# Performance work log

Measured on AMD Instinct MI355X. Metric: run time of the kernel, lower is better.

## Reference

```python
import jax, jax.numpy as jnp
import numpy as np

N_NODES = 50000
N_EDGES = 800000
F_NODE = 64
F_EDGE = 32
F_GLOBAL = 32
OUT_DIM = 64
N_GRAPHS = 256


def setup_inputs() -> dict:
    key = jax.random.key(0)
    ks = jax.random.split(key, 8)
    x = jax.random.normal(ks[0], (N_NODES, F_NODE), dtype=jnp.float32)
    edge_index = jax.random.randint(ks[1], (2, N_EDGES), 0, N_NODES, dtype=jnp.int64)
    edge_attr = jax.random.normal(ks[2], (N_EDGES, F_EDGE), dtype=jnp.float32)
    u = jax.random.normal(ks[3], (N_GRAPHS, F_GLOBAL), dtype=jnp.float32)
    batch = jnp.sort(jax.random.randint(ks[4], (N_NODES,), 0, N_GRAPHS, dtype=jnp.int64))
    # params (scaled like default Linear init)
    W1 = jax.random.normal(ks[5], (F_NODE + F_EDGE, OUT_DIM), dtype=jnp.float32) / np.sqrt(F_NODE + F_EDGE)
    b1 = jnp.zeros((OUT_DIM,), dtype=jnp.float32)
    W2 = jax.random.normal(ks[6], (F_NODE + OUT_DIM + F_GLOBAL, OUT_DIM), dtype=jnp.float32) / np.sqrt(F_NODE + OUT_DIM + F_GLOBAL)
    b2 = jnp.zeros((OUT_DIM,), dtype=jnp.float32)
    return {"x": x, "edge_index": edge_index, "edge_attr": edge_attr,
            "u": u, "batch": batch, "W1": W1, "b1": b1, "W2": W2, "b2": b2}


def reference(x, edge_index, edge_attr, u, batch, W1, b1, W2, b2):
    dest, src = edge_index[0], edge_index[1]
    # gather source node features + edge attrs -> [E, F_NODE + F_EDGE]
    edge_info = jnp.concatenate([x[src], edge_attr], axis=1)
    # node_mlp_1: Linear + ReLU
    edge_messages = jax.nn.relu(edge_info @ W1 + b1)  # [E, OUT_DIM]
    # scatter-sum into destination nodes
    aggregated = jax.ops.segment_sum(edge_messages, dest, num_segments=x.shape[0])  # [N, OUT_DIM]
    # concat node, aggregated messages, per-graph global
    node_info = jnp.concatenate([x, aggregated, u[batch]], axis=1)  # [N, F_NODE+OUT_DIM+F_GLOBAL]
    # node_mlp_2: Linear + ReLU
    return jax.nn.relu(node_info @ W2 + b2)  # [N, OUT_DIM]
```

## Files before the change

kernel.cpp:

```cpp
#include <hip/hip_runtime.h>
#include <hip/hip_bf16.h>
#include <hip/hip_fp16.h>

typedef __attribute__((ext_vector_type(8))) short short8;
typedef __attribute__((ext_vector_type(4))) float f32x4;

constexpr int NN = 50000;
constexpr int NE = 800000;
constexpr int FN = 64;
constexpr int FE = 32;
constexpr int FG = 32;
constexpr int OD = 64;
constexpr int NG = 256;

constexpr int SCAN_B = 256;
constexpr int NBLK = (NN + SCAN_B - 1) / SCAN_B;

constexpr int NWIN_E = NE / 16;
constexpr int MS_BLOCKS = 2048;
constexpr int MS_WAVES  = MS_BLOCKS * 4;
constexpr int NWIN_N = NN / 16;
constexpr int NODE_BLOCKS = 782;
constexpr int NODE_WAVES  = NODE_BLOCKS * 4;

static __device__ __forceinline__ unsigned pack_bf16(float a, float b) {
    __hip_bfloat162 h = __float22bfloat162_rn(float2{a, b});
    return *reinterpret_cast<unsigned*>(&h);
}

__global__ __launch_bounds__(256) void k_xcvt(const float* __restrict__ x,
                                              unsigned* __restrict__ xb32) {
    const int i = blockIdx.x * 256 + threadIdx.x;
    if (i >= NN * FN / 8) return;
    const float4* p = (const float4*)(x + (size_t)i * 8);
    float4 f0 = p[0], f1 = p[1];
    uint4 o;
    o.x = pack_bf16(f0.x, f0.y);
    o.y = pack_bf16(f0.z, f0.w);
    o.z = pack_bf16(f1.x, f1.y);
    o.w = pack_bf16(f1.z, f1.w);
    ((uint4*)xb32)[i] = o;
}

__global__ __launch_bounds__(256) void k_uw2(const float* __restrict__ u,
                                             const float* __restrict__ W2,
                                             const float* __restrict__ b2,
                                             float* __restrict__ uW2b) {
    const int lane = threadIdx.x & 63;
    float wcol[FG];
#pragma unroll
    for (int k = 0; k < FG; ++k) wcol[k] = W2[(FN + OD + k) * OD + lane];
    const float bias = b2[lane];

    int g = (blockIdx.x * blockDim.x + threadIdx.x) >> 6;
    g = __builtin_amdgcn_readfirstlane(g);
    if (g >= NG) return;

    const float* __restrict__ urow = u + (size_t)g * FG;
    float acc = bias;
#pragma unroll
    for (int k = 0; k < FG; ++k) acc = fmaf(urow[k], wcol[k], acc);
    uW2b[(size_t)g * OD + lane] = acc;
}

__global__ __launch_bounds__(256) void k_hist(const int* __restrict__ ei,
                                              int* __restrict__ cnt) {
    const int e = blockIdx.x * blockDim.x + threadIdx.x;
    if (e < NE) atomicAdd(&cnt[ei[e]], 1);
}

__global__ __launch_bounds__(SCAN_B) void k_scan1(const int* __restrict__ cnt,
                                                  int* __restrict__ start,
                                                  int* __restrict__ bsum) {
    __shared__ int lds[SCAN_B];
    const int i = blockIdx.x * SCAN_B + threadIdx.x;
    const int v = (i < NN) ? cnt[i] : 0;
    lds[threadIdx.x] = v;
    __syncthreads();
#pragma unroll
    for (int off = 1; off < SCAN_B; off <<= 1) {
        int t = (threadIdx.x >= off) ? lds[threadIdx.x - off] : 0;
        __syncthreads();
        lds[threadIdx.x] += t;
        __syncthreads();
    }
    const int incl = lds[threadIdx.x];
    if (i < NN) start[i] = incl - v;
    if (threadIdx.x == SCAN_B - 1) bsum[blockIdx.x] = incl;
}

__global__ __launch_bounds__(SCAN_B) void k_scan2(const int* __restrict__ bsum,
                                                  int* __restrict__ bscan) {
    __shared__ int lds[SCAN_B];
    const int i = threadIdx.x;
    const int v = (i < NBLK) ? bsum[i] : 0;
    lds[i] = v;
    __syncthreads();
#pragma unroll
    for (int off = 1; off < SCAN_B; off <<= 1) {
        int t = (i >= off) ? lds[i - off] : 0;
        __syncthreads();
        lds[i] += t;
        __syncthreads();
    }
    if (i < NBLK) bscan[i] = lds[i] - v;
}

__global__ __launch_bounds__(SCAN_B) void k_scan3(int* __restrict__ start,
                                                  const int* __restrict__ bscan,
                                                  const int* __restrict__ cnt,
                                                  int* __restrict__ cursor) {
    const int i = blockIdx.x * SCAN_B + threadIdx.x;
    if (i < NN) {
        const int s = start[i] + bscan[blockIdx.x];
        start[i] = s;
        cursor[i] = s;
        if (i == NN - 1) start[NN] = s + cnt[i];
    }
}

__global__ __launch_bounds__(256) void k_msgscat(const int* __restrict__ ei,
                                                 const float* __restrict__ ea,
                                                 const unsigned short* __restrict__ xb,
                                                 const float* __restrict__ W1,
                                                 const float* __restrict__ b1,
                                                 int* __restrict__ cursor,
                                                 unsigned short* __restrict__ mbuf) {
    const int l = threadIdx.x & 63;
    const int g = l >> 4;
    const int c = l & 15;

    short8 wf[3][4];
#pragma unroll
    for (int t = 0; t < 3; ++t)
#pragma unroll
        for (int b = 0; b < 4; ++b)
#pragma unroll
            for (int i = 0; i < 8; i += 2) {
                const int k = 32 * t + 8 * g + i;
                const unsigned p = pack_bf16(W1[k * OD + (c + 16 * b)],
                                             W1[(k + 1) * OD + (c + 16 * b)]);
                ((unsigned*)&wf[t][b])[i / 2] = p;
            }
    float bias[4];
#pragma unroll
    for (int b = 0; b < 4; ++b) bias[b] = b1[c + 16 * b];

    int wv = (blockIdx.x * blockDim.x + threadIdx.x) >> 6;
    wv = __builtin_amdgcn_readfirstlane(wv);

    for (int w = wv; w < NWIN_E; w += MS_WAVES) {
        const int e = w * 16 + c;
        const int dst = ei[e];
        const int src = ei[NE + e];
        int pos = 0;
        if (l < 16) pos = atomicAdd(&cursor[dst], 1);

        short8 a0, a1, a2;
        {
            const uint4* xr = (const uint4*)(xb + (size_t)src * FN);
            uint4 q0 = xr[g];
            uint4 q1 = xr[4 + g];
            a0 = *(short8*)&q0;
            a1 = *(short8*)&q1;
        }
        {
            const float4* er = (const float4*)(ea + (size_t)e * FE);
            float4 e0 = er[2 * g], e1 = er[2 * g + 1];
            uint4 q2;
            q2.x = pack_bf16(e0.x, e0.y);
            q2.y = pack_bf16(e0.z, e0.w);
            q2.z = pack_bf16(e1.x, e1.y);
            q2.w = pack_bf16(e1.z, e1.w);
            a2 = *(short8*)&q2;
        }

        f32x4 accb[4];
#pragma unroll
        for (int b = 0; b < 4; ++b) {
            f32x4 acc = {0.f, 0.f, 0.f, 0.f};
            acc = __builtin_amdgcn_mfma_f32_16x16x32_bf16(a0, wf[0][b], acc, 0, 0, 0);
            acc = __builtin_amdgcn_mfma_f32_16x16x32_bf16(a1, wf[1][b], acc, 0, 0, 0);
            acc = __builtin_amdgcn_mfma_f32_16x16x32_bf16(a2, wf[2][b], acc, 0, 0, 0);
            accb[b] = acc;
        }

#pragma unroll
        for (int q = 0; q < 4; ++q) {
            const int pr = __shfl(pos, 4 * g + q);
            const float v0 = fmaxf(accb[0][q] + bias[0], 0.0f);
            const float v1 = fmaxf(accb[1][q] + bias[1], 0.0f);
            const float v2 = fmaxf(accb[2][q] + bias[2], 0.0f);
            const float v3 = fmaxf(accb[3][q] + bias[3], 0.0f);
            const __half2 h01 = __float22half2_rn(float2{v0, v1});
            const __half2 h23 = __float22half2_rn(float2{v2, v3});
            uint2 out;
            out.x = *reinterpret_cast<const unsigned*>(&h01);
            out.y = *reinterpret_cast<const unsigned*>(&h23);
            *reinterpret_cast<uint2*>(mbuf + (size_t)pr * 64 + c * 4) = out;
        }
    }
}

__global__ __launch_bounds__(256) void k_segred(const unsigned short* __restrict__ mbuf,
                                                const int* __restrict__ start,
                                                unsigned short* __restrict__ aggb) {
    const int l = threadIdx.x & 63;
    int n = (blockIdx.x * blockDim.x + threadIdx.x) >> 6;
    n = __builtin_amdgcn_readfirstlane(n);
    if (n >= NN) return;

    const int r0 = start[n];
    const int r1 = start[n + 1];
    const __half* mh = (const __half*)mbuf;

    float s0 = 0.0f, s1 = 0.0f, s2 = 0.0f, s3 = 0.0f;
    int r = r0;
    for (; r + 3 < r1; r += 4) {
        s0 += __half2float(mh[(size_t)(r + 0) * 64 + l]);
        s1 += __half2float(mh[(size_t)(r + 1) * 64 + l]);
        s2 += __half2float(mh[(size_t)(r + 2) * 64 + l]);
        s3 += __half2float(mh[(size_t)(r + 3) * 64 + l]);
    }
    for (; r < r1; ++r) s0 += __half2float(mh[(size_t)r * 64 + l]);
    const float s = (s0 + s1) + (s2 + s3);

    const int tc = (l >> 2) + 16 * (l & 3);
    __hip_bfloat16 hb = __float2bfloat16(s);
    aggb[(size_t)n * OD + tc] = *reinterpret_cast<unsigned short*>(&hb);
}

__global__ __launch_bounds__(256) void k_nodem(const unsigned short* __restrict__ xb,
                                               const unsigned short* __restrict__ aggb,
                                               const int* __restrict__ bat,
                                               const float* __restrict__ uW2b,
                                               const float* __restrict__ W2,
                                               float* __restrict__ out) {
    const int l = threadIdx.x & 63;
    const int g = l >> 4;
    const int c = l & 15;

    short8 wf[4][4];
#pragma unroll
    for (int t = 0; t < 4; ++t)
#pragma unroll
        for (int b = 0; b < 4; ++b)
#pragma unroll
            for (int i = 0; i < 8; i += 2) {
                const int k = 32 * t + 8 * g + i;
                const unsigned p = pack_bf16(W2[k * OD + (c + 16 * b)],
                                             W2[(k + 1) * OD + (c + 16 * b)]);
                ((unsigned*)&wf[t][b])[i / 2] = p;
            }

    int wv = (blockIdx.x * blockDim.x + threadIdx.x) >> 6;
    wv = __builtin_amdgcn_readfirstlane(wv);

    for (int w = wv; w < NWIN_N; w += NODE_WAVES) {
        const int n0 = w * 16;
        const uint4* xr = (const uint4*)(xb + (size_t)(n0 + c) * FN);
        const uint4* ar = (const uint4*)(aggb + (size_t)(n0 + c) * OD);
        uint4 qx0 = xr[g], qx1 = xr[4 + g];
        uint4 qa0 = ar[g], qa1 = ar[4 + g];
        short8 a0 = *(short8*)&qx0, a1 = *(short8*)&qx1;
        short8 a2 = *(short8*)&qa0, a3 = *(short8*)&qa1;

        int bq[4];
#pragma unroll
        for (int q = 0; q < 4; ++q) bq[q] = bat[n0 + g * 4 + q];

#pragma unroll
        for (int b = 0; b < 4; ++b) {
            f32x4 acc = {0.f, 0.f, 0.f, 0.f};
            acc = __builtin_amdgcn_mfma_f32_16x16x32_bf16(a0, wf[0][b], acc, 0, 0, 0);
            acc = __builtin_amdgcn_mfma_f32_16x16x32_bf16(a1, wf[1][b], acc, 0, 0, 0);
            acc = __builtin_amdgcn_mfma_f32_16x16x32_bf16(a2, wf[2][b], acc, 0, 0, 0);
            acc = __builtin_amdgcn_mfma_f32_16x16x32_bf16(a3, wf[3][b], acc, 0, 0, 0);
#pragma unroll
            for (int q = 0; q < 4; ++q) {
                const int n = n0 + g * 4 + q;
                const float val = acc[q] + uW2b[(size_t)bq[q] * OD + c + 16 * b];
                out[(size_t)n * OD + c + 16 * b] = fmaxf(val, 0.0f);
            }
        }
    }
}

extern "C" void kernel_launch(void* const* d_in, const int* in_sizes, int n_in,
                              void* d_out, int out_size, void* d_ws, size_t ws_size,
                              hipStream_t stream) {
    const float* x    = (const float*)d_in[0];
    const int*   ei   = (const int*)d_in[1];
    const float* ea   = (const float*)d_in[2];
    const float* u    = (const float*)d_in[3];
    const int*   bat  = (const int*)d_in[4];
    const float* W1   = (const float*)d_in[5];
    const float* b1   = (const float*)d_in[6];
    const float* W2   = (const float*)d_in[7];
    const float* b2   = (const float*)d_in[8];
    float* out = (float*)d_out;

    char* ws = (char*)d_ws;
    auto alloc = [&](size_t bytes) {
        char* p = ws;
        ws += (bytes + 255) & ~size_t(255);
        return p;
    };
    unsigned short* xb   = (unsigned short*)alloc((size_t)NN * FN * 2);
    unsigned short* aggb = (unsigned short*)alloc((size_t)NN * OD * 2);
    float* uW2b    = (float*)alloc((size_t)NG * OD * sizeof(float));
    int*   cnt     = (int*)alloc((size_t)NN * sizeof(int));
    int*   start   = (int*)alloc((size_t)(NN + 1) * sizeof(int));
    int*   cursor  = (int*)alloc((size_t)NN * sizeof(int));
    int*   bsum    = (int*)alloc((size_t)NBLK * sizeof(int));
    int*   bscan   = (int*)alloc((size_t)NBLK * sizeof(int));
    unsigned short* mbuf = (unsigned short*)alloc((size_t)NE * OD * 2);

    hipMemsetAsync(cnt, 0, (size_t)NN * sizeof(int), stream);

    k_xcvt<<<dim3((NN * FN / 8 + 255) / 256), dim3(256), 0, stream>>>(x, (unsigned*)xb);
    k_uw2<<<dim3((NG * 64 + 255) / 256), dim3(256), 0, stream>>>(u, W2, b2, uW2b);

    k_hist<<<dim3((NE + 255) / 256), dim3(256), 0, stream>>>(ei, cnt);
    k_scan1<<<dim3(NBLK), dim3(SCAN_B), 0, stream>>>(cnt, start, bsum);
    k_scan2<<<dim3(1), dim3(SCAN_B), 0, stream>>>(bsum, bscan);
    k_scan3<<<dim3(NBLK), dim3(SCAN_B), 0, stream>>>(start, bscan, cnt, cursor);

    k_msgscat<<<dim3(MS_BLOCKS), dim3(256), 0, stream>>>(ei, ea, xb, W1, b1, cursor, mbuf);

    k_segred<<<dim3((NN * 64 + 255) / 256), dim3(256), 0, stream>>>(mbuf, start, aggb);

    k_nodem<<<dim3(NODE_BLOCKS), dim3(256), 0, stream>>>(xb, aggb, bat, uW2b, W2, out);
}
```

Measured before the change: 154.6 us.

## Precompute CSR slots in separate kernel; vectorize segment reduction with half2 loads

Moves the per-edge atomic cursor increment out of the MFMA message kernel into a new dedicated kernel that writes a slot index per edge. The message kernel then reads precomputed slots instead of doing atomics and shuffles. The segment reduction now loads half2 pairs, with two half-waves each taking alternate rows. This leaves the aggregate in a permuted column order, which is compensated by permuting the W2 rows loaded in the node kernel. The cost is an extra kernel launch plus writing and reading a 3.2MB slot array.

```diff
diff --git a/kernel.cpp b/kernel.cpp
--- a/kernel.cpp
+++ b/kernel.cpp
@@ -119,12 +119,22 @@
     }
 }
 
+__global__ __launch_bounds__(256) void k_slot(const int* __restrict__ ei,
+                                              int* __restrict__ cursor,
+                                              int* __restrict__ slotb) {
+    const int e = blockIdx.x * blockDim.x + threadIdx.x;
+    if (e < NE) {
+        const int pos = atomicAdd(&cursor[ei[e]], 1);
+        slotb[e] = pos;
+    }
+}
+
 __global__ __launch_bounds__(256) void k_msgscat(const int* __restrict__ ei,
                                                  const float* __restrict__ ea,
                                                  const unsigned short* __restrict__ xb,
                                                  const float* __restrict__ W1,
                                                  const float* __restrict__ b1,
-                                                 int* __restrict__ cursor,
+                                                 const int* __restrict__ slotb,
                                                  unsigned short* __restrict__ mbuf) {
     const int l = threadIdx.x & 63;
     const int g = l >> 4;
@@ -151,10 +161,11 @@
 
     for (int w = wv; w < NWIN_E; w += MS_WAVES) {
         const int e = w * 16 + c;
-        const int dst = ei[e];
         const int src = ei[NE + e];
-        int pos = 0;
-        if (l < 16) pos = atomicAdd(&cursor[dst], 1);
+
+        int pr[4];
+#pragma unroll
+        for (int q = 0; q < 4; ++q) pr[q] = slotb[w * 16 + 4 * g + q];
 
         short8 a0, a1, a2;
         {
@@ -187,7 +198,6 @@
 
 #pragma unroll
         for (int q = 0; q < 4; ++q) {
-            const int pr = __shfl(pos, 4 * g + q);
             const float v0 = fmaxf(accb[0][q] + bias[0], 0.0f);
             const float v1 = fmaxf(accb[1][q] + bias[1], 0.0f);
             const float v2 = fmaxf(accb[2][q] + bias[2], 0.0f);
@@ -197,37 +207,44 @@
             uint2 out;
             out.x = *reinterpret_cast<const unsigned*>(&h01);
             out.y = *reinterpret_cast<const unsigned*>(&h23);
-            *reinterpret_cast<uint2*>(mbuf + (size_t)pr * 64 + c * 4) = out;
-        }
-    }
-}
-
-__global__ __launch_bounds__(256) void k_segred(const unsigned short* __restrict__ mbuf,
+            *reinterpret_cast<uint2*>(mbuf + (size_t)pr[q] * 64 + c * 4) = out;
+        }
+    }
+}
+
+__global__ __launch_bounds__(256) void k_segred(const unsigned* __restrict__ mb32,
                                                 const int* __restrict__ start,
-                                                unsigned short* __restrict__ aggb) {
+                                                unsigned* __restrict__ aggb32) {
     const int l = threadIdx.x & 63;
+    const int half = l >> 5;
+    const int q = l & 31;
     int n = (blockIdx.x * blockDim.x + threadIdx.x) >> 6;
     n = __builtin_amdgcn_readfirstlane(n);
     if (n >= NN) return;
 
     const int r0 = start[n];
     const int r1 = start[n + 1];
-    const __half* mh = (const __half*)mbuf;
-
-    float s0 = 0.0f, s1 = 0.0f, s2 = 0.0f, s3 = 0.0f;
+
+    float c0 = 0.0f, c1 = 0.0f;
     int r = r0;
-    for (; r + 3 < r1; r += 4) {
-        s0 += __half2float(mh[(size_t)(r + 0) * 64 + l]);
-        s1 += __half2float(mh[(size_t)(r + 1) * 64 + l]);
-        s2 += __half2float(mh[(size_t)(r + 2) * 64 + l]);
-        s3 += __half2float(mh[(size_t)(r + 3) * 64 + l]);
-    }
-    for (; r < r1; ++r) s0 += __half2float(mh[(size_t)r * 64 + l]);
-    const float s = (s0 + s1) + (s2 + s3);
-
-    const int tc = (l >> 2) + 16 * (l & 3);
-    __hip_bfloat16 hb = __float2bfloat16(s);
-    aggb[(size_t)n * OD + tc] = *reinterpret_cast<unsigned short*>(&hb);
+#pragma unroll 4
+    for (; r + 1 < r1; r += 2) {
+        const unsigned uu = mb32[(size_t)(r + half) * 32 + q];
+        const __half2 h = *reinterpret_cast<const __half2*>(&uu);
+        const float2 f = __half22float2(h);
+        c0 += f.x;
+        c1 += f.y;
+    }
+    if (r < r1 && half == 0) {
+        const unsigned uu = mb32[(size_t)r * 32 + q];
+        const __half2 h = *reinterpret_cast<const __half2*>(&uu);
+        const float2 f = __half22float2(h);
+        c0 += f.x;
+        c1 += f.y;
+    }
+    c0 += __shfl_xor(c0, 32);
+    c1 += __shfl_xor(c1, 32);
+    if (half == 0) aggb32[(size_t)n * 32 + q] = pack_bf16(c0, c1);
 }
 
 __global__ __launch_bounds__(256) void k_nodem(const unsigned short* __restrict__ xb,
@@ -247,9 +264,18 @@
         for (int b = 0; b < 4; ++b)
 #pragma unroll
             for (int i = 0; i < 8; i += 2) {
-                const int k = 32 * t + 8 * g + i;
-                const unsigned p = pack_bf16(W2[k * OD + (c + 16 * b)],
-                                             W2[(k + 1) * OD + (c + 16 * b)]);
+                const int col = c + 16 * b;
+                unsigned p;
+                if (t < 2) {
+                    const int k = 32 * t + 8 * g + i;
+                    p = pack_bf16(W2[k * OD + col], W2[(k + 1) * OD + col]);
+                } else {
+                    const int sc0 = 32 * (t - 2) + 8 * g + i;
+                    const int sc1 = sc0 + 1;
+                    const int k0 = FN + ((sc0 >> 2) + 16 * (sc0 & 3));
+                    const int k1 = FN + ((sc1 >> 2) + 16 * (sc1 & 3));
+                    p = pack_bf16(W2[k0 * OD + col], W2[k1 * OD + col]);
+                }
                 ((unsigned*)&wf[t][b])[i / 2] = p;
             }
 
@@ -314,6 +340,7 @@
     int*   cursor  = (int*)alloc((size_t)NN * sizeof(int));
     int*   bsum    = (int*)alloc((size_t)NBLK * sizeof(int));
     int*   bscan   = (int*)alloc((size_t)NBLK * sizeof(int));
+    int*   slotb   = (int*)alloc((size_t)NE * sizeof(int));
     unsigned short* mbuf = (unsigned short*)alloc((size_t)NE * OD * 2);
 
     hipMemsetAsync(cnt, 0, (size_t)NN * sizeof(int), stream);
@@ -325,10 +352,11 @@
     k_scan1<<<dim3(NBLK), dim3(SCAN_B), 0, stream>>>(cnt, start, bsum);
     k_scan2<<<dim3(1), dim3(SCAN_B), 0, stream>>>(bsum, bscan);
     k_scan3<<<dim3(NBLK), dim3(SCAN_B), 0, stream>>>(start, bscan, cnt, cursor);
-
-    k_msgscat<<<dim3(MS_BLOCKS), dim3(256), 0, stream>>>(ei, ea, xb, W1, b1, cursor, mbuf);
-
-    k_segred<<<dim3((NN * 64 + 255) / 256), dim3(256), 0, stream>>>(mbuf, start, aggb);
+    k_slot<<<dim3((NE + 255) / 256), dim3(256), 0, stream>>>(ei, cursor, slotb);
+
+    k_msgscat<<<dim3(MS_BLOCKS), dim3(256), 0, stream>>>(ei, ea, xb, W1, b1, slotb, mbuf);
+
+    k_segred<<<dim3((NN * 64 + 255) / 256), dim3(256), 0, stream>>>((const unsigned*)mbuf, start, (unsigned*)aggb);
 
     k_nodem<<<dim3(NODE_BLOCKS), dim3(256), 0, stream>>>(xb, aggb, bat, uW2b, W2, out);
 }
```

Result: slower. 179.5 us (+16.1%).

## Fuse segment reduction into node MLP and merge small preprocessing kernels

Applied to the files above, without the earlier changes.

Removes the separate segment-reduce kernel. Each node-MLP wave now sums its 16 nodes' fp16 messages directly from the sorted message buffer into bf16 MFMA operands, and the W2 aggregate rows are permuted to match the lane layout. The x conversion, u·W2 precompute and count zeroing are merged into one kernel, and the two scan tail kernels become one that rescans the block sums redundantly in every block. This cuts launches and the aggregate write/read round trip. The cost is load imbalance inside each wave, since every node's loop runs to the maximum degree among its 16 nodes.

```diff
diff --git a/kernel.cpp b/kernel.cpp
--- a/kernel.cpp
+++ b/kernel.cpp
@@ -19,6 +19,10 @@
 constexpr int NWIN_E = NE / 16;
 constexpr int MS_BLOCKS = 2048;
 constexpr int MS_WAVES  = MS_BLOCKS * 4;
+
+constexpr int XCVT_BLOCKS = (NN * FN / 8 + 255) / 256;
+constexpr int PRE_BLOCKS  = XCVT_BLOCKS + (NG * 64) / 256;
+
 constexpr int NWIN_N = NN / 16;
 constexpr int NODE_BLOCKS = 782;
 constexpr int NODE_WAVES  = NODE_BLOCKS * 4;
@@ -28,9 +32,31 @@
     return *reinterpret_cast<unsigned*>(&h);
 }
 
-__global__ __launch_bounds__(256) void k_xcvt(const float* __restrict__ x,
-                                              unsigned* __restrict__ xb32) {
+__global__ __launch_bounds__(256) void k_pre(const float* __restrict__ x,
+                                             unsigned* __restrict__ xb32,
+                                             const float* __restrict__ u,
+                                             const float* __restrict__ W2,
+                                             const float* __restrict__ b2,
+                                             float* __restrict__ uW2b,
+                                             int* __restrict__ cnt) {
+    if (blockIdx.x >= XCVT_BLOCKS) {
+        const int lane = threadIdx.x & 63;
+        float wcol[FG];
+#pragma unroll
+        for (int k = 0; k < FG; ++k) wcol[k] = W2[(FN + OD + k) * OD + lane];
+        const float bias = b2[lane];
+        int g = ((blockIdx.x - XCVT_BLOCKS) * 256 + threadIdx.x) >> 6;
+        g = __builtin_amdgcn_readfirstlane(g);
+        if (g >= NG) return;
+        const float* __restrict__ urow = u + (size_t)g * FG;
+        float acc = bias;
+#pragma unroll
+        for (int k = 0; k < FG; ++k) acc = fmaf(urow[k], wcol[k], acc);
+        uW2b[(size_t)g * OD + lane] = acc;
+        return;
+    }
     const int i = blockIdx.x * 256 + threadIdx.x;
+    if (i < NN) cnt[i] = 0;
     if (i >= NN * FN / 8) return;
     const float4* p = (const float4*)(x + (size_t)i * 8);
     float4 f0 = p[0], f1 = p[1];
@@ -42,27 +68,6 @@
     ((uint4*)xb32)[i] = o;
 }
 
-__global__ __launch_bounds__(256) void k_uw2(const float* __restrict__ u,
-                                             const float* __restrict__ W2,
-                                             const float* __restrict__ b2,
-                                             float* __restrict__ uW2b) {
-    const int lane = threadIdx.x & 63;
-    float wcol[FG];
-#pragma unroll
-    for (int k = 0; k < FG; ++k) wcol[k] = W2[(FN + OD + k) * OD + lane];
-    const float bias = b2[lane];
-
-    int g = (blockIdx.x * blockDim.x + threadIdx.x) >> 6;
-    g = __builtin_amdgcn_readfirstlane(g);
-    if (g >= NG) return;
-
-    const float* __restrict__ urow = u + (size_t)g * FG;
-    float acc = bias;
-#pragma unroll
-    for (int k = 0; k < FG; ++k) acc = fmaf(urow[k], wcol[k], acc);
-    uW2b[(size_t)g * OD + lane] = acc;
-}
-
 __global__ __launch_bounds__(256) void k_hist(const int* __restrict__ ei,
                                               int* __restrict__ cnt) {
     const int e = blockIdx.x * blockDim.x + threadIdx.x;
@@ -89,30 +94,26 @@
     if (threadIdx.x == SCAN_B - 1) bsum[blockIdx.x] = incl;
 }
 
-__global__ __launch_bounds__(SCAN_B) void k_scan2(const int* __restrict__ bsum,
-                                                  int* __restrict__ bscan) {
+__global__ __launch_bounds__(SCAN_B) void k_scan23(int* __restrict__ start,
+                                                   const int* __restrict__ bsum,
+                                                   const int* __restrict__ cnt,
+                                                   int* __restrict__ cursor) {
     __shared__ int lds[SCAN_B];
-    const int i = threadIdx.x;
-    const int v = (i < NBLK) ? bsum[i] : 0;
-    lds[i] = v;
+    const int t = threadIdx.x;
+    lds[t] = (t < NBLK) ? bsum[t] : 0;
     __syncthreads();
 #pragma unroll
     for (int off = 1; off < SCAN_B; off <<= 1) {
-        int t = (i >= off) ? lds[i - off] : 0;
+        int tv = (t >= off) ? lds[t - off] : 0;
         __syncthreads();
-        lds[i] += t;
+        lds[t] += tv;
         __syncthreads();
     }
-    if (i < NBLK) bscan[i] = lds[i] - v;
-}
-
-__global__ __launch_bounds__(SCAN_B) void k_scan3(int* __restrict__ start,
-                                                  const int* __restrict__ bscan,
-                                                  const int* __restrict__ cnt,
-                                                  int* __restrict__ cursor) {
-    const int i = blockIdx.x * SCAN_B + threadIdx.x;
+    const int boff = (blockIdx.x == 0) ? 0 : lds[blockIdx.x - 1];
+
+    const int i = blockIdx.x * SCAN_B + t;
     if (i < NN) {
-        const int s = start[i] + bscan[blockIdx.x];
+        const int s = start[i] + boff;
         start[i] = s;
         cursor[i] = s;
         if (i == NN - 1) start[NN] = s + cnt[i];
@@ -194,48 +195,21 @@
             const float v3 = fmaxf(accb[3][q] + bias[3], 0.0f);
             const __half2 h01 = __float22half2_rn(float2{v0, v1});
             const __half2 h23 = __float22half2_rn(float2{v2, v3});
-            uint2 out;
-            out.x = *reinterpret_cast<const unsigned*>(&h01);
-            out.y = *reinterpret_cast<const unsigned*>(&h23);
-            *reinterpret_cast<uint2*>(mbuf + (size_t)pr * 64 + c * 4) = out;
-        }
-    }
-}
-
-__global__ __launch_bounds__(256) void k_segred(const unsigned short* __restrict__ mbuf,
+            uint2 outv;
+            outv.x = *reinterpret_cast<const unsigned*>(&h01);
+            outv.y = *reinterpret_cast<const unsigned*>(&h23);
+            *reinterpret_cast<uint2*>(mbuf + (size_t)pr * 64 + c * 4) = outv;
+        }
+    }
+}
+
+__global__ __launch_bounds__(256) void k_nodem2(const unsigned short* __restrict__ xb,
+                                                const unsigned short* __restrict__ mbuf,
                                                 const int* __restrict__ start,
-                                                unsigned short* __restrict__ aggb) {
-    const int l = threadIdx.x & 63;
-    int n = (blockIdx.x * blockDim.x + threadIdx.x) >> 6;
-    n = __builtin_amdgcn_readfirstlane(n);
-    if (n >= NN) return;
-
-    const int r0 = start[n];
-    const int r1 = start[n + 1];
-    const __half* mh = (const __half*)mbuf;
-
-    float s0 = 0.0f, s1 = 0.0f, s2 = 0.0f, s3 = 0.0f;
-    int r = r0;
-    for (; r + 3 < r1; r += 4) {
-        s0 += __half2float(mh[(size_t)(r + 0) * 64 + l]);
-        s1 += __half2float(mh[(size_t)(r + 1) * 64 + l]);
-        s2 += __half2float(mh[(size_t)(r + 2) * 64 + l]);
-        s3 += __half2float(mh[(size_t)(r + 3) * 64 + l]);
-    }
-    for (; r < r1; ++r) s0 += __half2float(mh[(size_t)r * 64 + l]);
-    const float s = (s0 + s1) + (s2 + s3);
-
-    const int tc = (l >> 2) + 16 * (l & 3);
-    __hip_bfloat16 hb = __float2bfloat16(s);
-    aggb[(size_t)n * OD + tc] = *reinterpret_cast<unsigned short*>(&hb);
-}
-
-__global__ __launch_bounds__(256) void k_nodem(const unsigned short* __restrict__ xb,
-                                               const unsigned short* __restrict__ aggb,
-                                               const int* __restrict__ bat,
-                                               const float* __restrict__ uW2b,
-                                               const float* __restrict__ W2,
-                                               float* __restrict__ out) {
+                                                const int* __restrict__ bat,
+                                                const float* __restrict__ uW2b,
+                                                const float* __restrict__ W2,
+                                                float* __restrict__ out) {
     const int l = threadIdx.x & 63;
     const int g = l >> 4;
     const int c = l & 15;
@@ -247,9 +221,18 @@
         for (int b = 0; b < 4; ++b)
 #pragma unroll
             for (int i = 0; i < 8; i += 2) {
-                const int k = 32 * t + 8 * g + i;
-                const unsigned p = pack_bf16(W2[k * OD + (c + 16 * b)],
-                                             W2[(k + 1) * OD + (c + 16 * b)]);
+                const int col = c + 16 * b;
+                unsigned p;
+                if (t < 2) {
+                    const int k = 32 * t + 8 * g + i;
+                    p = pack_bf16(W2[k * OD + col], W2[(k + 1) * OD + col]);
+                } else {
+                    const int sc0 = 32 * (t - 2) + 8 * g + i;
+                    const int sc1 = sc0 + 1;
+                    const int k0 = FN + ((sc0 >> 2) + 16 * (sc0 & 3));
+                    const int k1 = FN + ((sc1 >> 2) + 16 * (sc1 & 3));
+                    p = pack_bf16(W2[k0 * OD + col], W2[k1 * OD + col]);
+                }
                 ((unsigned*)&wf[t][b])[i / 2] = p;
             }
 
@@ -258,12 +241,50 @@
 
     for (int w = wv; w < NWIN_N; w += NODE_WAVES) {
         const int n0 = w * 16;
-        const uint4* xr = (const uint4*)(xb + (size_t)(n0 + c) * FN);
-        const uint4* ar = (const uint4*)(aggb + (size_t)(n0 + c) * OD);
+        const int n = n0 + c;
+        const int s0 = start[n];
+        const int cntn = start[n + 1] - s0;
+
+        int mc = cntn;
+        mc = max(mc, __shfl_xor(mc, 1));
+        mc = max(mc, __shfl_xor(mc, 2));
+        mc = max(mc, __shfl_xor(mc, 4));
+        mc = max(mc, __shfl_xor(mc, 8));
+
+        float s2v[8] = {0, 0, 0, 0, 0, 0, 0, 0};
+        float s3v[8] = {0, 0, 0, 0, 0, 0, 0, 0};
+        const unsigned short* rowb = mbuf + (size_t)s0 * 64 + 8 * g;
+        for (int i = 0; i < mc; ++i) {
+            if (i < cntn) {
+                const uint4 u2 = *(const uint4*)(rowb + (size_t)i * 64);
+                const uint4 u3 = *(const uint4*)(rowb + (size_t)i * 64 + 32);
+                const __half2* h2 = (const __half2*)&u2;
+                const __half2* h3 = (const __half2*)&u3;
+#pragma unroll
+                for (int j = 0; j < 4; ++j) {
+                    const float2 f2 = __half22float2(h2[j]);
+                    const float2 f3 = __half22float2(h3[j]);
+                    s2v[2 * j]     += f2.x;
+                    s2v[2 * j + 1] += f2.y;
+                    s3v[2 * j]     += f3.x;
+                    s3v[2 * j + 1] += f3.y;
+                }
+            }
+        }
+        uint4 qa2, qa3;
+        qa2.x = pack_bf16(s2v[0], s2v[1]);
+        qa2.y = pack_bf16(s2v[2], s2v[3]);
+        qa2.z = pack_bf16(s2v[4], s2v[5]);
+        qa2.w = pack_bf16(s2v[6], s2v[7]);
+        qa3.x = pack_bf16(s3v[0], s3v[1]);
+        qa3.y = pack_bf16(s3v[2], s3v[3]);
+        qa3.z = pack_bf16(s3v[4], s3v[5]);
+        qa3.w = pack_bf16(s3v[6], s3v[7]);
+
+        const uint4* xr = (const uint4*)(xb + (size_t)n * FN);
         uint4 qx0 = xr[g], qx1 = xr[4 + g];
-        uint4 qa0 = ar[g], qa1 = ar[4 + g];
         short8 a0 = *(short8*)&qx0, a1 = *(short8*)&qx1;
-        short8 a2 = *(short8*)&qa0, a3 = *(short8*)&qa1;
+        short8 a2 = *(short8*)&qa2, a3 = *(short8*)&qa3;
 
         int bq[4];
 #pragma unroll
@@ -278,9 +299,9 @@
             acc = __builtin_amdgcn_mfma_f32_16x16x32_bf16(a3, wf[3][b], acc, 0, 0, 0);
 #pragma unroll
             for (int q = 0; q < 4; ++q) {
-                const int n = n0 + g * 4 + q;
+                const int nn = n0 + g * 4 + q;
                 const float val = acc[q] + uW2b[(size_t)bq[q] * OD + c + 16 * b];
-                out[(size_t)n * OD + c + 16 * b] = fmaxf(val, 0.0f);
+                out[(size_t)nn * OD + c + 16 * b] = fmaxf(val, 0.0f);
             }
         }
     }
@@ -306,29 +327,21 @@
         ws += (bytes + 255) & ~size_t(255);
         return p;
     };
-    unsigned short* xb   = (unsigned short*)alloc((size_t)NN * FN * 2);
-    unsigned short* aggb = (unsigned short*)alloc((size_t)NN * OD * 2);
+    unsigned short* xb = (unsigned short*)alloc((size_t)NN * FN * 2);
     float* uW2b    = (float*)alloc((size_t)NG * OD * sizeof(float));
     int*   cnt     = (int*)alloc((size_t)NN * sizeof(int));
     int*   start   = (int*)alloc((size_t)(NN + 1) * sizeof(int));
     int*   cursor  = (int*)alloc((size_t)NN * sizeof(int));
     int*   bsum    = (int*)alloc((size_t)NBLK * sizeof(int));
-    int*   bscan   = (int*)alloc((size_t)NBLK * sizeof(int));
     unsigned short* mbuf = (unsigned short*)alloc((size_t)NE * OD * 2);
 
-    hipMemsetAsync(cnt, 0, (size_t)NN * sizeof(int), stream);
-
-    k_xcvt<<<dim3((NN * FN / 8 + 255) / 256), dim3(256), 0, stream>>>(x, (unsigned*)xb);
-    k_uw2<<<dim3((NG * 64 + 255) / 256), dim3(256), 0, stream>>>(u, W2, b2, uW2b);
+    k_pre<<<dim3(PRE_BLOCKS), dim3(256), 0, stream>>>(x, (unsigned*)xb, u, W2, b2, uW2b, cnt);
 
     k_hist<<<dim3((NE + 255) / 256), dim3(256), 0, stream>>>(ei, cnt);
     k_scan1<<<dim3(NBLK), dim3(SCAN_B), 0, stream>>>(cnt, start, bsum);
-    k_scan2<<<dim3(1), dim3(SCAN_B), 0, stream>>>(bsum, bscan);
-    k_scan3<<<dim3(NBLK), dim3(SCAN_B), 0, stream>>>(start, bscan, cnt, cursor);
+    k_scan23<<<dim3(NBLK), dim3(SCAN_B), 0, stream>>>(start, bsum, cnt, cursor);
 
     k_msgscat<<<dim3(MS_BLOCKS), dim3(256), 0, stream>>>(ei, ea, xb, W1, b1, cursor, mbuf);
 
-    k_segred<<<dim3((NN * 64 + 255) / 256), dim3(256), 0, stream>>>(mbuf, start, aggb);
-
-    k_nodem<<<dim3(NODE_BLOCKS), dim3(256), 0, stream>>>(xb, aggb, bat, uW2b, W2, out);
-}
+    k_nodem2<<<dim3(NODE_BLOCKS), dim3(256), 0, stream>>>(xb, mbuf, start, bat, uW2b, W2, out);
+}
```

Result: faster. 149.7 us (median of 3 runs) (-3.2%).
